# Performance work log

Hardware: AMD Instinct MI355X
Metric: run time of the kernel (lower is better)

The kernel has to match this reference:

```python
import jax, jax.numpy as jnp
import numpy as np

B, T, C, H = 4, 4096, 1024, 64  # batch, seq_len, embedding_dimension, head_size


def setup_inputs() -> dict:
    key = jax.random.key(0)
    kx, kq, kk, kv = jax.random.split(key, 4)
    x = jax.random.normal(kx, (B, T, C), dtype=jnp.float32)
    # nn.Linear(C, H, bias=False) -> weight applied as x @ W with W:[C,H]
    s = 1.0 / np.sqrt(C)
    Wq = jax.random.normal(kq, (C, H), dtype=jnp.float32) * s
    Wk = jax.random.normal(kk, (C, H), dtype=jnp.float32) * s
    Wv = jax.random.normal(kv, (C, H), dtype=jnp.float32) * s
    return {"x": x, "Wq": Wq, "Wk": Wk, "Wv": Wv}


def reference(x, Wq, Wk, Wv):
    Bx, Tx, Cx = x.shape
    q = x @ Wq  # [B,T,H]
    k = x @ Wk  # [B,T,H]
    v = x @ Wv  # [B,T,H]
    # NOTE: original scales by C**-0.5 (embedding dim), not head_size**-0.5
    wei = jnp.einsum('bqh,bkh->bqk', q, k) * (Cx ** -0.5)  # [B,T,T]
    causal = jnp.tril(jnp.ones((Tx, Tx), dtype=bool))
    wei = jnp.where(causal, wei, -jnp.inf)
    wei = jax.nn.softmax(wei, axis=-1)
    out = jnp.einsum('bqk,bkh->bqh', wei, v)  # [B,T,H]
    return out
```

## Files before the change

kernel.cpp:

```cpp
#include <hip/hip_runtime.h>
#include <math.h>

#define BATCH 4
#define SEQ   4096
#define EMB   1024
#define HDIM  64
#define NSPLIT 4

typedef __attribute__((ext_vector_type(8))) short bf16x8;
typedef __attribute__((ext_vector_type(4))) float f32x4;
typedef __attribute__((ext_vector_type(4))) unsigned int u32x4;

#define MFMA16(a, b, c) __builtin_amdgcn_mfma_f32_16x16x32_bf16(a, b, c, 0, 0, 0)

__device__ __forceinline__ unsigned short f2bf(float f) {
  unsigned int u = __float_as_uint(f);
  u = (u + 0x7FFFu + ((u >> 16) & 1u)) >> 16;
  return (unsigned short)u;
}

__device__ __forceinline__ float fexp2(float x) {
  float r;
  asm("v_exp_f32 %0, %1" : "=v"(r) : "v"(x));
  return r;
}

__global__ __launch_bounds__(256) void wt_kernel(
    const float* __restrict__ Wq, const float* __restrict__ Wk,
    const float* __restrict__ Wv, unsigned short* __restrict__ wt) {
  __shared__ float tile[64][65];
  const int bid = blockIdx.x;
  const int m = bid >> 4, kt = bid & 15;
  const float* W = (m == 0) ? Wq : (m == 1) ? Wk : Wv;
  const int tid = threadIdx.x;
  {
    const int r = tid >> 2, c4 = tid & 3;
    const float* src = W + (size_t)(kt * 64 + r) * 64 + c4 * 16;
#pragma unroll
    for (int j = 0; j < 4; ++j) {
      float4 a = *(const float4*)(src + j * 4);
      tile[r][c4 * 16 + j * 4 + 0] = a.x;
      tile[r][c4 * 16 + j * 4 + 1] = a.y;
      tile[r][c4 * 16 + j * 4 + 2] = a.z;
      tile[r][c4 * 16 + j * 4 + 3] = a.w;
    }
  }
  __syncthreads();
  {
    const int col = tid >> 2, kq = tid & 3;
    unsigned short o[16];
#pragma unroll
    for (int j = 0; j < 16; ++j) o[j] = f2bf(tile[kq * 16 + j][col]);
    unsigned short* dst = wt + (size_t)(m * 64 + col) * 1024 + kt * 64 + kq * 16;
    *(bf16x8*)(dst)     = *(bf16x8*)&o[0];
    *(bf16x8*)(dst + 8) = *(bf16x8*)&o[8];
  }
}

__global__ __launch_bounds__(256) void qkv_mfma_kernel(
    const float* __restrict__ x, const unsigned short* __restrict__ wt,
    unsigned short* __restrict__ qb, unsigned short* __restrict__ kb,
    unsigned short* __restrict__ vt) {
  __shared__ __align__(16) unsigned short xs[32 * 64];
  __shared__ __align__(16) unsigned short ws[192 * 64];
  const int tid  = threadIdx.x;
  const int lane = tid & 63, wid = tid >> 6;
  const int g = lane >> 4, p = lane & 15;
  const size_t row0 = (size_t)blockIdx.x * 32;

  const int sr = tid >> 3, sc = tid & 7;
  const float* xp = x + (row0 + sr) * EMB + sc * 8;

  f32x4 acc[2][3];
#pragma unroll
  for (int rt = 0; rt < 2; ++rt)
#pragma unroll
    for (int ct = 0; ct < 3; ++ct) acc[rt][ct] = (f32x4){0.f, 0.f, 0.f, 0.f};

  float4 rx[2];
  bf16x8 rw[6];
#pragma unroll
  for (int j = 0; j < 2; ++j) rx[j] = *(const float4*)(xp + j * 4);
#pragma unroll
  for (int it = 0; it < 6; ++it) {
    int i = tid + it * 256, col = i >> 3, cc = i & 7;
    rw[it] = *(const bf16x8*)(wt + (size_t)col * 1024 + cc * 8);
  }

  for (int kc = 0; kc < 16; ++kc) {
    __syncthreads();
#pragma unroll
    for (int j = 0; j < 2; ++j) {
      ushort4 h;
      h.x = f2bf(rx[j].x); h.y = f2bf(rx[j].y);
      h.z = f2bf(rx[j].z); h.w = f2bf(rx[j].w);
      *(ushort4*)((char*)xs + ((sr * 128 + sc * 16 + j * 8) ^ ((sr & 7) << 4))) = h;
    }
#pragma unroll
    for (int it = 0; it < 6; ++it) {
      int i = tid + it * 256, col = i >> 3, cc = i & 7;
      *(bf16x8*)((char*)ws + ((col * 128 + cc * 16) ^ ((col & 7) << 4))) = rw[it];
    }
    if (kc < 15) {
      const float* xpn = xp + (kc + 1) * 64;
#pragma unroll
      for (int j = 0; j < 2; ++j) rx[j] = *(const float4*)(xpn + j * 4);
#pragma unroll
      for (int it = 0; it < 6; ++it) {
        int i = tid + it * 256, col = i >> 3, cc = i & 7;
        rw[it] = *(const bf16x8*)(wt + (size_t)col * 1024 + (kc + 1) * 64 + cc * 8);
      }
    }
    __syncthreads();
#pragma unroll
    for (int ks = 0; ks < 2; ++ks) {
      bf16x8 af[2];
#pragma unroll
      for (int rt = 0; rt < 2; ++rt) {
        int row = rt * 16 + p;
        af[rt] = *(const bf16x8*)((char*)xs +
                 ((row * 128 + ks * 64 + g * 16) ^ ((row & 7) << 4)));
      }
#pragma unroll
      for (int ct = 0; ct < 3; ++ct) {
        int col = wid * 48 + ct * 16 + p;
        bf16x8 bfr = *(const bf16x8*)((char*)ws +
                     ((col * 128 + ks * 64 + g * 16) ^ ((col & 7) << 4)));
#pragma unroll
        for (int rt = 0; rt < 2; ++rt)
          acc[rt][ct] = MFMA16(af[rt], bfr, acc[rt][ct]);
      }
    }
  }

  const int b     = (int)(row0 >> 12);
  const int tbase = (int)(row0 & 4095);
  unsigned short* vtb = vt + (((size_t)b * 64 + (tbase >> 6)) * 64) * 64 + (tbase & 63);
#pragma unroll
  for (int rt = 0; rt < 2; ++rt)
#pragma unroll
    for (int ct = 0; ct < 3; ++ct) {
      const int c0  = wid * 48 + ct * 16;
      const int mtx = c0 >> 6;
      const int col = (c0 & 63) + p;
#pragma unroll
      for (int r = 0; r < 4; ++r) {
        const int row = rt * 16 + 4 * g + r;
        const float vf = acc[rt][ct][r];
        if (mtx == 0)      qb[(row0 + row) * HDIM + col] = f2bf(vf * 0.0450843714f);
        else if (mtx == 1) kb[(row0 + row) * HDIM + col] = f2bf(vf);
        else               vtb[(size_t)col * 64 + row]   = f2bf(vf);
      }
    }
}

__device__ __forceinline__ void tile_body_lds(
    const unsigned short* __restrict__ sKb, const unsigned short* __restrict__ sVb,
    int qrel, bool diag,
    const bf16x8& qf0, const bf16x8& qf1,
    int p, int g, int cA0, int cA1, int srcA, int srcB, bool hi,
    float& m, float& l, f32x4 (&o)[4]) {
  f32x4 sc4[4];
#pragma unroll
  for (int t = 0; t < 4; ++t) {
    const int row = 16 * t + p;
    bf16x8 a0 = *(const bf16x8*)((const char*)sKb + row * 128 + cA0);
    bf16x8 a1 = *(const bf16x8*)((const char*)sKb + row * 128 + cA1);
    f32x4 a = (f32x4){0.f, 0.f, 0.f, 0.f};
    a = MFMA16(a0, qf0, a);
    a = MFMA16(a1, qf1, a);
    sc4[t] = a;
  }
  if (diag) {
#pragma unroll
    for (int t = 0; t < 4; ++t)
#pragma unroll
      for (int r = 0; r < 4; ++r)
        if (16 * t + 4 * g + r > qrel) sc4[t][r] = -1e30f;
  }
  float tm = -3e38f;
#pragma unroll
  for (int t = 0; t < 4; ++t)
#pragma unroll
    for (int r = 0; r < 4; ++r) tm = fmaxf(tm, sc4[t][r]);
  tm = fmaxf(tm, __shfl_xor(tm, 16));
  tm = fmaxf(tm, __shfl_xor(tm, 32));
  if (__any(tm > m + 11.5f)) {
    float mn = fmaxf(m, tm);
    float c = fexp2(m - mn);
    l *= c;
#pragma unroll
    for (int mi = 0; mi < 4; ++mi) o[mi] *= c;
    m = mn;
  }
  float psum = 0.f;
#pragma unroll
  for (int t = 0; t < 4; ++t)
#pragma unroll
    for (int r = 0; r < 4; ++r) {
      float pv = fexp2(sc4[t][r] - m);
      sc4[t][r] = pv;
      psum += pv;
    }
  l += psum;
  unsigned int pk[4][2];
#pragma unroll
  for (int t = 0; t < 4; ++t) {
    asm("v_cvt_pk_bf16_f32 %0, %1, %2"
        : "=v"(pk[t][0]) : "v"(sc4[t][0]), "v"(sc4[t][1]));
    asm("v_cvt_pk_bf16_f32 %0, %1, %2"
        : "=v"(pk[t][1]) : "v"(sc4[t][2]), "v"(sc4[t][3]));
  }
  u32x4 wb0, wb1;
#pragma unroll
  for (int h2 = 0; h2 < 2; ++h2) {
    const int src = h2 ? srcB : srcA;
    unsigned c0 = (unsigned)__shfl((int)pk[0][0], src);
    unsigned c1 = (unsigned)__shfl((int)pk[1][0], src);
    wb0[2 * h2 + 0] = hi ? c1 : c0;
    unsigned d0 = (unsigned)__shfl((int)pk[0][1], src);
    unsigned d1 = (unsigned)__shfl((int)pk[1][1], src);
    wb0[2 * h2 + 1] = hi ? d1 : d0;
    unsigned e0 = (unsigned)__shfl((int)pk[2][0], src);
    unsigned e1 = (unsigned)__shfl((int)pk[3][0], src);
    wb1[2 * h2 + 0] = hi ? e1 : e0;
    unsigned f0 = (unsigned)__shfl((int)pk[2][1], src);
    unsigned f1 = (unsigned)__shfl((int)pk[3][1], src);
    wb1[2 * h2 + 1] = hi ? f1 : f0;
  }
  bf16x8 b0 = __builtin_bit_cast(bf16x8, wb0);
  bf16x8 b1 = __builtin_bit_cast(bf16x8, wb1);
#pragma unroll
  for (int mi = 0; mi < 4; ++mi) {
    const int rowv = 16 * mi + p;
    bf16x8 va0 = *(const bf16x8*)((const char*)sVb + rowv * 128 + cA0);
    bf16x8 va1 = *(const bf16x8*)((const char*)sVb + rowv * 128 + cA1);
    o[mi] = MFMA16(va0, b0, o[mi]);
    o[mi] = MFMA16(va1, b1, o[mi]);
  }
}

__device__ __forceinline__ void item_map(int g_it, int j, int& kt, bool& isA, bool& diag) {
  if (g_it <= j) { isA = true;  kt = g_it;         diag = (g_it == j); }
  else           { isA = false; kt = g_it - j - 1; diag = (kt == 63 - j); }
}

__global__ __launch_bounds__(256) void attn_partial_kernel(
    const unsigned short* __restrict__ qb, const unsigned short* __restrict__ kbm,
    const unsigned short* __restrict__ vt, float* __restrict__ pw) {
  __shared__ __align__(16) unsigned short sK[2][4096];
  __shared__ __align__(16) unsigned short sV[2][4096];
  const int tid = threadIdx.x;
  const int wid = tid >> 6, lane = tid & 63;
  const int g = lane >> 4, p = lane & 15;
  const int bid = blockIdx.x;
  const int sp = bid & 3, j = (bid >> 2) & 31, b = bid >> 7;
  const int jB = 63 - j;
  const int tq0A = j * 64 + 16 * wid;
  const int tq0B = jB * 64 + 16 * wid;

  const char* kbase = (const char*)(kbm + (size_t)b * SEQ * HDIM);
  const char* vbase = (const char*)(vt  + (size_t)b * SEQ * HDIM);

  const unsigned short* qrowA = qb + ((size_t)b * SEQ + tq0A + p) * HDIM;
  const bf16x8 qfA0 = *(const bf16x8*)(qrowA + 8 * g);
  const bf16x8 qfA1 = *(const bf16x8*)(qrowA + 32 + 8 * g);
  const unsigned short* qrowB = qb + ((size_t)b * SEQ + tq0B + p) * HDIM;
  const bf16x8 qfB0 = *(const bf16x8*)(qrowB + 8 * g);
  const bf16x8 qfB1 = *(const bf16x8*)(qrowB + 32 + 8 * g);

  const int slot0 = tid * 16, slot1 = slot0 + 4096;
  const int r0 = slot0 >> 7, koff0 = r0 * 128 + ((slot0 & 127) ^ ((r0 & 7) << 4));
  const int r1 = slot1 >> 7, koff1 = r1 * 128 + ((slot1 & 127) ^ ((r1 & 7) << 4));

  const int swz = (p & 7) << 4;
  const int cA0 = (16 * g) ^ swz, cA1 = (64 + 16 * g) ^ swz;

  const int srcA = (g & 1) * 32 + p;
  const int srcB = srcA + 16;
  const bool hi = (g >> 1) != 0;

  float mA = -1e30f, lA = 0.f, mB = -1e30f, lB = 0.f;
  f32x4 oA[4], oB[4];
#pragma unroll
  for (int mi = 0; mi < 4; ++mi) {
    oA[mi] = (f32x4){0.f, 0.f, 0.f, 0.f};
    oB[mi] = (f32x4){0.f, 0.f, 0.f, 0.f};
  }

  const int cnt = (65 - sp + NSPLIT - 1) / NSPLIT;

  bf16x8 rk0, rk1, rv0, rv1;
  {
    int kt; bool isA, diag;
    item_map(sp, j, kt, isA, diag);
    const char* kk = kbase + (size_t)kt * 8192;
    const char* vv = vbase + (size_t)kt * 8192;
    rk0 = *(const bf16x8*)(kk + koff0); rk1 = *(const bf16x8*)(kk + koff1);
    rv0 = *(const bf16x8*)(vv + koff0); rv1 = *(const bf16x8*)(vv + koff1);
  }

  for (int ii = 0; ii < cnt; ++ii) {
    const int buf = ii & 1;
    __syncthreads();
    *(bf16x8*)((char*)sK[buf] + slot0) = rk0;
    *(bf16x8*)((char*)sK[buf] + slot1) = rk1;
    *(bf16x8*)((char*)sV[buf] + slot0) = rv0;
    *(bf16x8*)((char*)sV[buf] + slot1) = rv1;
    if (ii + 1 < cnt) {
      int kt; bool isA, diag;
      item_map(sp + (ii + 1) * NSPLIT, j, kt, isA, diag);
      const char* kk = kbase + (size_t)kt * 8192;
      const char* vv = vbase + (size_t)kt * 8192;
      rk0 = *(const bf16x8*)(kk + koff0); rk1 = *(const bf16x8*)(kk + koff1);
      rv0 = *(const bf16x8*)(vv + koff0); rv1 = *(const bf16x8*)(vv + koff1);
    }
    __syncthreads();
    int kt; bool isA, diag;
    item_map(sp + ii * NSPLIT, j, kt, isA, diag);
    if (isA) {
      tile_body_lds(sK[buf], sV[buf], tq0A + p - kt * 64, diag, qfA0, qfA1,
                    p, g, cA0, cA1, srcA, srcB, hi, mA, lA, oA);
    } else {
      tile_body_lds(sK[buf], sV[buf], tq0B + p - kt * 64, diag, qfB0, qfB1,
                    p, g, cA0, cA1, srcA, srcB, hi, mB, lB, oB);
    }
  }

  lA += __shfl_xor(lA, 16); lA += __shfl_xor(lA, 32);
  lB += __shfl_xor(lB, 16); lB += __shfl_xor(lB, 32);

  {
    const int grpA = j * 4 + wid;
    float* pp = pw + ((size_t)(b * 256 + grpA) * NSPLIT + sp) * 1056;
#pragma unroll
    for (int mi = 0; mi < 4; ++mi)
      *(f32x4*)(pp + p * 64 + 16 * mi + 4 * g) = oA[mi];
    if (g == 0) { pp[1024 + p] = mA; pp[1040 + p] = lA; }
  }
  {
    const int grpB = jB * 4 + wid;
    float* pp = pw + ((size_t)(b * 256 + grpB) * NSPLIT + sp) * 1056;
#pragma unroll
    for (int mi = 0; mi < 4; ++mi)
      *(f32x4*)(pp + p * 64 + 16 * mi + 4 * g) = oB[mi];
    if (g == 0) { pp[1024 + p] = mB; pp[1040 + p] = lB; }
  }
}

__global__ __launch_bounds__(256) void attn_merge_kernel(
    const float* __restrict__ pw, float* __restrict__ out) {
  const int bid = blockIdx.x;
  const int b = bid >> 8, grp = bid & 255;
  const int q = threadIdx.x & 15, db = threadIdx.x >> 4;
  const float* pp = pw + (size_t)bid * NSPLIT * 1056;
  float ms[NSPLIT], ls[NSPLIT];
  float mm = -3e38f;
#pragma unroll
  for (int s = 0; s < NSPLIT; ++s) {
    ms[s] = pp[s * 1056 + 1024 + q];
    ls[s] = pp[s * 1056 + 1040 + q];
    mm = fmaxf(mm, ms[s]);
  }
  float L = 0.f, a0 = 0.f, a1 = 0.f, a2 = 0.f, a3 = 0.f;
#pragma unroll
  for (int s = 0; s < NSPLIT; ++s) {
    float sc = fexp2(ms[s] - mm);
    L += ls[s] * sc;
    float4 v = *(const float4*)(pp + s * 1056 + q * 64 + 4 * db);
    a0 += v.x * sc; a1 += v.y * sc; a2 += v.z * sc; a3 += v.w * sc;
  }
  const float inv = 1.f / L;
  float* op = out + ((size_t)b * SEQ + grp * 16 + q) * HDIM + 4 * db;
  op[0] = a0 * inv; op[1] = a1 * inv; op[2] = a2 * inv; op[3] = a3 * inv;
}

extern "C" void kernel_launch(void* const* d_in, const int* in_sizes, int n_in,
                              void* d_out, int out_size, void* d_ws, size_t ws_size,
                              hipStream_t stream) {
  const float* x  = (const float*)d_in[0];
  const float* Wq = (const float*)d_in[1];
  const float* Wk = (const float*)d_in[2];
  const float* Wv = (const float*)d_in[3];
  float* outp = (float*)d_out;

  const size_t rows = (size_t)BATCH * SEQ;
  unsigned short* qbf = (unsigned short*)d_ws;
  unsigned short* kbf = qbf + rows * HDIM;
  unsigned short* vtb = kbf + rows * HDIM;
  unsigned short* wt  = vtb + rows * HDIM;
  float* pw = (float*)(wt + 192 * 1024);

  wt_kernel<<<dim3(48), dim3(256), 0, stream>>>(Wq, Wk, Wv, wt);
  qkv_mfma_kernel<<<dim3((unsigned)(rows / 32)), dim3(256), 0, stream>>>(x, wt, qbf, kbf, vtb);
  attn_partial_kernel<<<dim3(512), dim3(256), 0, stream>>>(qbf, kbf, vtb, pw);
  attn_merge_kernel<<<dim3(1024), dim3(256), 0, stream>>>(pw, outp);
}
```

Before: 61.59 us.

## Fuse split-KV merge into attention kernel via last-block atomic counter

Removes the separate merge kernel launch. Each attention block bumps an atomic counter for its (batch, query-pair) after writing its partials, and the last of the four split blocks merges all eight query groups and writes the output. The counters are zeroed in the weight-transpose kernel. This saves a launch and its gap, in exchange for a serialized tail merge inside the last blocks plus threadfence and atomic overhead.

```diff
diff --git a/kernel.cpp b/kernel.cpp
--- a/kernel.cpp
+++ b/kernel.cpp
@@ -27,12 +27,14 @@
 
 __global__ __launch_bounds__(256) void wt_kernel(
     const float* __restrict__ Wq, const float* __restrict__ Wk,
-    const float* __restrict__ Wv, unsigned short* __restrict__ wt) {
+    const float* __restrict__ Wv, unsigned short* __restrict__ wt,
+    int* __restrict__ cnt) {
   __shared__ float tile[64][65];
   const int bid = blockIdx.x;
   const int m = bid >> 4, kt = bid & 15;
   const float* W = (m == 0) ? Wq : (m == 1) ? Wk : Wv;
   const int tid = threadIdx.x;
+  if (bid == 0 && tid < 128) cnt[tid] = 0;
   {
     const int r = tid >> 2, c4 = tid & 3;
     const float* src = W + (size_t)(kt * 64 + r) * 64 + c4 * 16;
@@ -247,9 +249,11 @@
 
 __global__ __launch_bounds__(256) void attn_partial_kernel(
     const unsigned short* __restrict__ qb, const unsigned short* __restrict__ kbm,
-    const unsigned short* __restrict__ vt, float* __restrict__ pw) {
+    const unsigned short* __restrict__ vt, float* __restrict__ pw,
+    int* __restrict__ cnt, float* __restrict__ out) {
   __shared__ __align__(16) unsigned short sK[2][4096];
   __shared__ __align__(16) unsigned short sV[2][4096];
+  __shared__ int lastf;
   const int tid = threadIdx.x;
   const int wid = tid >> 6, lane = tid & 63;
   const int g = lane >> 4, p = lane & 15;
@@ -288,7 +292,7 @@
     oB[mi] = (f32x4){0.f, 0.f, 0.f, 0.f};
   }
 
-  const int cnt = (65 - sp + NSPLIT - 1) / NSPLIT;
+  const int cntN = (65 - sp + NSPLIT - 1) / NSPLIT;
 
   bf16x8 rk0, rk1, rv0, rv1;
   {
@@ -300,14 +304,14 @@
     rv0 = *(const bf16x8*)(vv + koff0); rv1 = *(const bf16x8*)(vv + koff1);
   }
 
-  for (int ii = 0; ii < cnt; ++ii) {
+  for (int ii = 0; ii < cntN; ++ii) {
     const int buf = ii & 1;
     __syncthreads();
     *(bf16x8*)((char*)sK[buf] + slot0) = rk0;
     *(bf16x8*)((char*)sK[buf] + slot1) = rk1;
     *(bf16x8*)((char*)sV[buf] + slot0) = rv0;
     *(bf16x8*)((char*)sV[buf] + slot1) = rv1;
-    if (ii + 1 < cnt) {
+    if (ii + 1 < cntN) {
       int kt; bool isA, diag;
       item_map(sp + (ii + 1) * NSPLIT, j, kt, isA, diag);
       const char* kk = kbase + (size_t)kt * 8192;
@@ -346,33 +350,39 @@
       *(f32x4*)(pp + p * 64 + 16 * mi + 4 * g) = oB[mi];
     if (g == 0) { pp[1024 + p] = mB; pp[1040 + p] = lB; }
   }
-}
-
-__global__ __launch_bounds__(256) void attn_merge_kernel(
-    const float* __restrict__ pw, float* __restrict__ out) {
-  const int bid = blockIdx.x;
-  const int b = bid >> 8, grp = bid & 255;
-  const int q = threadIdx.x & 15, db = threadIdx.x >> 4;
-  const float* pp = pw + (size_t)bid * NSPLIT * 1056;
-  float ms[NSPLIT], ls[NSPLIT];
-  float mm = -3e38f;
-#pragma unroll
-  for (int s = 0; s < NSPLIT; ++s) {
-    ms[s] = pp[s * 1056 + 1024 + q];
-    ls[s] = pp[s * 1056 + 1040 + q];
-    mm = fmaxf(mm, ms[s]);
-  }
-  float L = 0.f, a0 = 0.f, a1 = 0.f, a2 = 0.f, a3 = 0.f;
-#pragma unroll
-  for (int s = 0; s < NSPLIT; ++s) {
-    float sc = fexp2(ms[s] - mm);
-    L += ls[s] * sc;
-    float4 v = *(const float4*)(pp + s * 1056 + q * 64 + 4 * db);
-    a0 += v.x * sc; a1 += v.y * sc; a2 += v.z * sc; a3 += v.w * sc;
-  }
-  const float inv = 1.f / L;
-  float* op = out + ((size_t)b * SEQ + grp * 16 + q) * HDIM + 4 * db;
-  op[0] = a0 * inv; op[1] = a1 * inv; op[2] = a2 * inv; op[3] = a3 * inv;
+
+  __threadfence();
+  __syncthreads();
+  if (tid == 0) lastf = (atomicAdd(&cnt[b * 32 + j], 1) == 3);
+  __syncthreads();
+  if (lastf) {
+    __threadfence();
+    const int q = tid & 15, db = tid >> 4;
+#pragma unroll
+    for (int gi = 0; gi < 8; ++gi) {
+      const int grp = (gi < 4) ? (j * 4 + gi) : (jB * 4 + (gi - 4));
+      const float* pp = pw + ((size_t)(b * 256 + grp) * NSPLIT) * 1056;
+      float ms[NSPLIT], ls[NSPLIT];
+      float mm = -3e38f;
+#pragma unroll
+      for (int s = 0; s < NSPLIT; ++s) {
+        ms[s] = pp[s * 1056 + 1024 + q];
+        ls[s] = pp[s * 1056 + 1040 + q];
+        mm = fmaxf(mm, ms[s]);
+      }
+      float L = 0.f, a0 = 0.f, a1 = 0.f, a2 = 0.f, a3 = 0.f;
+#pragma unroll
+      for (int s = 0; s < NSPLIT; ++s) {
+        float sc = fexp2(ms[s] - mm);
+        L += ls[s] * sc;
+        float4 v = *(const float4*)(pp + s * 1056 + q * 64 + 4 * db);
+        a0 += v.x * sc; a1 += v.y * sc; a2 += v.z * sc; a3 += v.w * sc;
+      }
+      const float inv = 1.f / L;
+      float* op = out + ((size_t)b * SEQ + grp * 16 + q) * HDIM + 4 * db;
+      op[0] = a0 * inv; op[1] = a1 * inv; op[2] = a2 * inv; op[3] = a3 * inv;
+    }
+  }
 }
 
 extern "C" void kernel_launch(void* const* d_in, const int* in_sizes, int n_in,
@@ -390,9 +400,9 @@
   unsigned short* vtb = kbf + rows * HDIM;
   unsigned short* wt  = vtb + rows * HDIM;
   float* pw = (float*)(wt + 192 * 1024);
-
-  wt_kernel<<<dim3(48), dim3(256), 0, stream>>>(Wq, Wk, Wv, wt);
+  int* cnt  = (int*)(pw + (size_t)4096 * 1056);
+
+  wt_kernel<<<dim3(48), dim3(256), 0, stream>>>(Wq, Wk, Wv, wt, cnt);
   qkv_mfma_kernel<<<dim3((unsigned)(rows / 32)), dim3(256), 0, stream>>>(x, wt, qbf, kbf, vtb);
-  attn_partial_kernel<<<dim3(512), dim3(256), 0, stream>>>(qbf, kbf, vtb, pw);
-  attn_merge_kernel<<<dim3(1024), dim3(256), 0, stream>>>(pw, outp);
-}
+  attn_partial_kernel<<<dim3(512), dim3(256), 0, stream>>>(qbf, kbf, vtb, pw, cnt, outp);
+}
```

Measured after the change: 172.1 us. +179.5%, slower.
